# Optimization experiments

Measured on AMD Instinct MI355X. Metric: run time of the kernel, lower is better.

## Reference

```python
import jax, jax.numpy as jnp
import numpy as np

N_NODES = 4096  # nodes per graph (output1 reshaped to [-1, N_NODES])


def setup_inputs() -> dict:
    key = jax.random.key(0)
    ks = jax.random.split(key, 10)
    total_nodes = 64 * N_NODES          # 64 graphs of 4096 nodes
    n_edges = total_nodes * 8           # avg degree 8 lattice-like graph
    n_hidden = 128
    return {
        "node_features": jax.random.normal(ks[0], (total_nodes, 1), jnp.float32),
        "src": jax.random.randint(ks[1], (n_edges,), 0, total_nodes, jnp.int32),
        "dst": jax.random.randint(ks[2], (n_edges,), 0, total_nodes, jnp.int32),
        "w_self1": jax.random.normal(ks[3], (1, n_hidden), jnp.float32) * 0.5,
        "w_neigh1": jax.random.normal(ks[4], (1, n_hidden), jnp.float32) * 0.5,
        "b1": jnp.zeros((n_hidden,), jnp.float32),
        "w_self2": jax.random.normal(ks[5], (n_hidden, 1), jnp.float32) * (1.0 / np.sqrt(n_hidden)),
        "w_neigh2": jax.random.normal(ks[6], (n_hidden, 1), jnp.float32) * (1.0 / np.sqrt(n_hidden)),
        "b2": jnp.zeros((1,), jnp.float32),
        "w3": jax.random.normal(ks[7], (N_NODES, N_NODES), jnp.float32) * (1.0 / np.sqrt(N_NODES)),
        "b3": jnp.zeros((N_NODES,), jnp.float32),
    }


def _sage_mean(feat, src, dst, w_self, w_neigh, b, num_nodes):
    # gather source-node features along edges, mean-reduce at destination
    agg = jax.ops.segment_sum(feat[src], dst, num_segments=num_nodes)
    deg = jax.ops.segment_sum(jnp.ones((src.shape[0], 1), feat.dtype), dst,
                              num_segments=num_nodes)
    h_neigh = agg / jnp.maximum(deg, 1.0)
    return feat @ w_self + h_neigh @ w_neigh + b


def reference(node_features, src, dst, w_self1, w_neigh1, b1,
              w_self2, w_neigh2, b2, w3, b3):
    n = node_features.shape[0]
    h1 = jnp.tanh(_sage_mean(node_features, src, dst, w_self1, w_neigh1, b1, n))
    out1 = _sage_mean(h1, src, dst, w_self2, w_neigh2, b2, n)
    output1 = out1.reshape(-1, N_NODES)          # [batch, n_nodes]
    h2 = jnp.tanh(output1)
    output2 = h2 @ w3 + b3
    return (output1, output2)
```

## Files before the change

### kernel.cpp

```cpp
#include <hip/hip_runtime.h>


#define NTOT (64 * 4096)
#define NHID 128
#define GK   4096
#define KCH  256
#define KCHUNKS 16
#define NBINS 128
#define BSZ   2048
#define BSH   11
#define CAP   17408
#define NSL   4
#define SCB   256

typedef unsigned int u32;

__device__ __forceinline__ float fast_tanh(float x) {
    float ax = fabsf(x);
    float t  = __expf(-2.0f * ax);
    float r  = (1.0f - t) / (1.0f + t);
    return copysignf(r, x);
}


__global__ void __launch_bounds__(1024) scatter_x(const int* __restrict__ src,
                                                  const int* __restrict__ dst,
                                                  int n_edges,
                                                  int* __restrict__ edge_cnt,
                                                  u32* __restrict__ packed) {
    __shared__ int lc[NBINS];
    __shared__ int lbase[NBINS];
    int t = threadIdx.x;
    if (t < NBINS) lc[t] = 0;
    __syncthreads();
    int per = (n_edges + gridDim.x - 1) / gridDim.x;
    int e0 = blockIdx.x * per;
    int e1 = min(e0 + per, n_edges);

    int dreg[8], sreg[8];
#pragma unroll
    for (int i = 0; i < 8; ++i) {
        int e = e0 + t + i * 1024;
        bool ok = e < e1;
        int d = ok ? dst[e] : -1;
        dreg[i] = d;
        sreg[i] = ok ? src[e] : 0;
        if (ok) atomicAdd(&lc[d >> BSH], 1);
    }
    __syncthreads();
    if (t < NBINS) {
        lbase[t] = atomicAdd(&edge_cnt[t], lc[t]);
        lc[t] = 0;
    }
    __syncthreads();
#pragma unroll
    for (int i = 0; i < 8; ++i) {
        int d = dreg[i];
        if (d >= 0) {
            int b = d >> BSH;
            int pos = lbase[b] + atomicAdd(&lc[b], 1);
            if (pos < CAP)
                packed[(size_t)b * CAP + pos] =
                    ((u32)(d & (BSZ - 1)) << 18) | (u32)sreg[i];
        }
    }
}

__global__ void __launch_bounds__(1024) agg1_x(const u32* __restrict__ packed,
                                               const int* __restrict__ edge_cnt,
                                               const float* __restrict__ nf,
                                               float* __restrict__ part1) {
    __shared__ float lsum[BSZ];
    __shared__ float lcnt[BSZ];
    int t = threadIdx.x;
    int b = blockIdx.x, s = blockIdx.y;
    for (int i = t; i < BSZ; i += 1024) { lsum[i] = 0.0f; lcnt[i] = 0.0f; }
    __syncthreads();
    int en  = min(edge_cnt[b], CAP);
    int per = (en + NSL - 1) / NSL;
    int e0  = s * per;
    int e1  = min(e0 + per, en);
    const u32* pk = packed + (size_t)b * CAP;
    for (int e = e0 + t; e < e1; e += 1024) {
        u32 p = pk[e];
        int local = (int)(p >> 18);
        atomicAdd(&lsum[local], nf[p & 0x3FFFFu]);
        atomicAdd(&lcnt[local], 1.0f);
    }
    __syncthreads();
    float* dp = part1 + ((size_t)(b * NSL + s) * 2) * BSZ;
    for (int i = t; i < BSZ; i += 1024) { dp[i] = lsum[i]; dp[BSZ + i] = lcnt[i]; }
}

__global__ void node1_x(const float* __restrict__ nf, const float* __restrict__ part1,
                        const float* __restrict__ w_s1, const float* __restrict__ w_n1,
                        const float* __restrict__ bb1,
                        const float* __restrict__ w_s2, const float* __restrict__ w_n2,
                        float* __restrict__ degf, float* __restrict__ selfp,
                        float* __restrict__ sp) {
    __shared__ float lws1[NHID], lwn1[NHID], lb1[NHID], lws2[NHID], lwn2[NHID];
    int tid = threadIdx.x;
    if (tid < NHID) {
        lws1[tid] = w_s1[tid];
        lwn1[tid] = w_n1[tid];
        lb1[tid]  = bb1[tid];
        lws2[tid] = w_s2[tid];
        lwn2[tid] = w_n2[tid];
    }
    __syncthreads();
    int v = blockIdx.x * blockDim.x + tid;
    int b = v >> BSH, local = v & (BSZ - 1);
    float sum = 0.0f, cf = 0.0f;
#pragma unroll
    for (int s = 0; s < NSL; ++s) {
        const float* dp = part1 + ((size_t)(b * NSL + s) * 2) * BSZ;
        sum += dp[local];
        cf  += dp[BSZ + local];
    }
    float hn = sum / fmaxf(cf, 1.0f);
    float f = nf[v];
    float a = 0.0f, s2 = 0.0f;
#pragma unroll 8
    for (int j = 0; j < NHID; ++j) {
        float t = fast_tanh(fmaf(f, lws1[j], fmaf(hn, lwn1[j], lb1[j])));
        a  = fmaf(t, lws2[j], a);
        s2 = fmaf(t, lwn2[j], s2);
    }
    degf[v]  = cf;
    selfp[v] = a;
    sp[v]    = s2;
}

__global__ void __launch_bounds__(1024) agg2_x(const u32* __restrict__ packed,
                                               const int* __restrict__ edge_cnt,
                                               const float* __restrict__ spv,
                                               float* __restrict__ part2) {
    __shared__ float lsum[BSZ];
    int t = threadIdx.x;
    int b = blockIdx.x, s = blockIdx.y;
    for (int i = t; i < BSZ; i += 1024) lsum[i] = 0.0f;
    __syncthreads();
    int en  = min(edge_cnt[b], CAP);
    int per = (en + NSL - 1) / NSL;
    int e0  = s * per;
    int e1  = min(e0 + per, en);
    const u32* pk = packed + (size_t)b * CAP;
    for (int e = e0 + t; e < e1; e += 1024) {
        u32 p = pk[e];
        atomicAdd(&lsum[p >> 18], spv[p & 0x3FFFFu]);
    }
    __syncthreads();
    float* dp = part2 + (size_t)(b * NSL + s) * BSZ;
    for (int i = t; i < BSZ; i += 1024) dp[i] = lsum[i];
}

__global__ void node2_x(const float* __restrict__ selfp, const float* __restrict__ part2,
                        const float* __restrict__ degf, const float* __restrict__ b2p,
                        float* __restrict__ out1, float* __restrict__ h2t) {
    int v = blockIdx.x * blockDim.x + threadIdx.x;
    int b = v >> BSH, local = v & (BSZ - 1);
    float agg2 = 0.0f;
#pragma unroll
    for (int s = 0; s < NSL; ++s)
        agg2 += part2[(size_t)(b * NSL + s) * BSZ + local];
    float o = selfp[v] + agg2 / fmaxf(degf[v], 1.0f) + b2p[0];
    out1[v] = o;
    int r = v >> 12;
    int k = v & 4095;
    h2t[k * 64 + r] = fast_tanh(o);
}

__global__ void __launch_bounds__(512, 4) gemm_x(const float* __restrict__ h2t,
                                                 const float* __restrict__ w3,
                                                 float* __restrict__ Cpart) {
    int lane = threadIdx.x & 63;
    int wv   = threadIdx.x >> 6;
    int colb = blockIdx.x * 128 + lane * 2;
    int k0   = blockIdx.y * KCH;
    int row0 = __builtin_amdgcn_readfirstlane(wv * 8);

    const float* Ap = h2t + (size_t)k0 * 64 + row0;
    const float* wp = w3 + (size_t)k0 * GK + colb;

    float2 acc[8];
#pragma unroll
    for (int r = 0; r < 8; ++r) { acc[r].x = 0.0f; acc[r].y = 0.0f; }

    float2 bvA[8], bvB[8];
    float  avA[8], avB[8];

#pragma unroll
    for (int j = 0; j < 8; ++j) bvA[j] = *(const float2*)(wp + (size_t)j * GK);
#pragma unroll
    for (int r = 0; r < 8; ++r) avA[r] = Ap[r];

    for (int kk = 0; kk < KCH; kk += 16) {
#pragma unroll
        for (int j = 0; j < 8; ++j)
            bvB[j] = *(const float2*)(wp + (size_t)(kk + 8 + j) * GK);
#pragma unroll
        for (int j = 0; j < 8; ++j) {
            const float* An = Ap + (size_t)(kk + j + 1) * 64;
            float2 b = bvA[j];
            if ((j & 1) == 0) {
#pragma unroll
                for (int r = 0; r < 8; ++r) avB[r] = An[r];
#pragma unroll
                for (int r = 0; r < 8; ++r) {
                    acc[r].x = fmaf(avA[r], b.x, acc[r].x);
                    acc[r].y = fmaf(avA[r], b.y, acc[r].y);
                }
            } else {
#pragma unroll
                for (int r = 0; r < 8; ++r) avA[r] = An[r];
#pragma unroll
                for (int r = 0; r < 8; ++r) {
                    acc[r].x = fmaf(avB[r], b.x, acc[r].x);
                    acc[r].y = fmaf(avB[r], b.y, acc[r].y);
                }
            }
        }
        if (kk + 16 < KCH) {
#pragma unroll
            for (int j = 0; j < 8; ++j)
                bvA[j] = *(const float2*)(wp + (size_t)(kk + 16 + j) * GK);
        }
#pragma unroll
        for (int j = 0; j < 8; ++j) {
            int kn = kk + 8 + j + 1;
            if (kn > KCH - 1) kn = KCH - 1;
            const float* An = Ap + (size_t)kn * 64;
            float2 b = bvB[j];
            if ((j & 1) == 0) {
#pragma unroll
                for (int r = 0; r < 8; ++r) avB[r] = An[r];
#pragma unroll
                for (int r = 0; r < 8; ++r) {
                    acc[r].x = fmaf(avA[r], b.x, acc[r].x);
                    acc[r].y = fmaf(avA[r], b.y, acc[r].y);
                }
            } else {
#pragma unroll
                for (int r = 0; r < 8; ++r) avA[r] = An[r];
#pragma unroll
                for (int r = 0; r < 8; ++r) {
                    acc[r].x = fmaf(avB[r], b.x, acc[r].x);
                    acc[r].y = fmaf(avB[r], b.y, acc[r].y);
                }
            }
        }
    }

    float* Cp = Cpart + (size_t)blockIdx.y * NTOT + (size_t)row0 * GK + colb;
#pragma unroll
    for (int r = 0; r < 8; ++r) *(float2*)(Cp + (size_t)r * GK) = acc[r];
}

__global__ void reduce_x(const float4* __restrict__ Cpart, const float4* __restrict__ b3v,
                         float4* __restrict__ out2) {
    int v = blockIdx.x * blockDim.x + threadIdx.x;
    float4 s = b3v[v & 1023];
#pragma unroll
    for (int kc = 0; kc < KCHUNKS; ++kc) {
        float4 c = Cpart[(size_t)kc * (NTOT / 4) + v];
        s.x += c.x; s.y += c.y; s.z += c.z; s.w += c.w;
    }
    out2[v] = s;
}


__global__ void edge_pass1_f(const int* __restrict__ src, const int* __restrict__ dst,
                             const float* __restrict__ nf, float* __restrict__ agg,
                             float* __restrict__ deg, int n_edges) {
    int e = blockIdx.x * blockDim.x + threadIdx.x;
    if (e >= n_edges) return;
    int s = src[e], d = dst[e];
    atomicAdd(&agg[d], nf[s]);
    atomicAdd(&deg[d], 1.0f);
}

__global__ void node1_f(const float* __restrict__ nf, float* s0,
                        const float* __restrict__ deg,
                        const float* __restrict__ w_s1, const float* __restrict__ w_n1,
                        const float* __restrict__ bb1,
                        const float* __restrict__ w_s2, const float* __restrict__ w_n2,
                        float* __restrict__ sp) {
    __shared__ float lws1[NHID], lwn1[NHID], lb1[NHID], lws2[NHID], lwn2[NHID];
    int tid = threadIdx.x;
    if (tid < NHID) {
        lws1[tid] = w_s1[tid];
        lwn1[tid] = w_n1[tid];
        lb1[tid]  = bb1[tid];
        lws2[tid] = w_s2[tid];
        lwn2[tid] = w_n2[tid];
    }
    __syncthreads();
    int v = blockIdx.x * blockDim.x + tid;
    float f  = nf[v];
    float hn = s0[v] / fmaxf(deg[v], 1.0f);
    float a = 0.0f, s = 0.0f;
#pragma unroll 8
    for (int j = 0; j < NHID; ++j) {
        float t = fast_tanh(fmaf(f, lws1[j], fmaf(hn, lwn1[j], lb1[j])));
        a = fmaf(t, lws2[j], a);
        s = fmaf(t, lwn2[j], s);
    }
    s0[v] = a;
    sp[v] = s;
}

__global__ void edge_pass2_f(const int* __restrict__ src, const int* __restrict__ dst,
                             const float* __restrict__ sp, float* __restrict__ agg2,
                             int n_edges) {
    int e = blockIdx.x * blockDim.x + threadIdx.x;
    if (e >= n_edges) return;
    atomicAdd(&agg2[dst[e]], sp[src[e]]);
}

__global__ void node2_f(const float* __restrict__ s0, const float* __restrict__ agg2,
                        const float* __restrict__ deg, const float* __restrict__ b2p,
                        const float* __restrict__ b3p,
                        float* __restrict__ out1, float* __restrict__ h2t,
                        float* __restrict__ out2) {
    int v = blockIdx.x * blockDim.x + threadIdx.x;
    float o = s0[v] + agg2[v] / fmaxf(deg[v], 1.0f) + b2p[0];
    out1[v] = o;
    int r = v >> 12;
    int k = v & 4095;
    h2t[k * 64 + r] = fast_tanh(o);
    out2[v] = b3p[v & 4095];
}

__global__ void __launch_bounds__(256) gemm_f(const float* __restrict__ h2t,
                                              const float* __restrict__ w3,
                                              float* __restrict__ out2) {
    int n  = blockIdx.x * 256 + threadIdx.x;
    int k0 = blockIdx.y * KCH;
    float acc[64];
#pragma unroll
    for (int r = 0; r < 64; ++r) acc[r] = 0.0f;
    for (int k = k0; k < k0 + KCH; ++k) {
        float bv = w3[(size_t)k * GK + n];
        const float* Ak = h2t + k * 64;
#pragma unroll
        for (int r = 0; r < 64; ++r) acc[r] = fmaf(Ak[r], bv, acc[r]);
    }
#pragma unroll
    for (int r = 0; r < 64; ++r) atomicAdd(&out2[r * GK + n], acc[r]);
}


extern "C" void kernel_launch(void* const* d_in, const int* in_sizes, int n_in,
                              void* d_out, int out_size, void* d_ws, size_t ws_size,
                              hipStream_t stream) {
    const float* nf  = (const float*)d_in[0];
    const int*   src = (const int*)d_in[1];
    const int*   dst = (const int*)d_in[2];
    const float* ws1 = (const float*)d_in[3];
    const float* wn1 = (const float*)d_in[4];
    const float* b1  = (const float*)d_in[5];
    const float* ws2 = (const float*)d_in[6];
    const float* wn2 = (const float*)d_in[7];
    const float* b2  = (const float*)d_in[8];
    const float* w3  = (const float*)d_in[9];
    const float* b3  = (const float*)d_in[10];
    float* out1 = (float*)d_out;
    float* out2 = (float*)d_out + NTOT;

    int n_edges = in_sizes[1];
    int eb = (n_edges + 255) / 256;

    if (ws_size >= (size_t)20 * 1024 * 1024 && n_edges <= (1 << 21)) {
        char*  base     = (char*)d_ws;
        u32*   packed   = (u32*)base;
        float* part     = (float*)(base + 8912896);
        float* degf     = (float*)(base + 17301504);
        float* selfp    = (float*)(base + 18350080);
        float* spbuf    = (float*)(base + 19398656);
        int*   edge_cnt = (int*)(base + 20447232);
        float* h2t      = spbuf;
        float* Cpart    = (float*)base;

        (void)hipMemsetAsync(edge_cnt, 0, NBINS * sizeof(int), stream);
        scatter_x<<<SCB, 1024, 0, stream>>>(src, dst, n_edges, edge_cnt, packed);
        agg1_x<<<dim3(NBINS, NSL), 1024, 0, stream>>>(packed, edge_cnt, nf, part);
        node1_x<<<NTOT / 256, 256, 0, stream>>>(nf, part, ws1, wn1, b1, ws2, wn2,
                                                degf, selfp, spbuf);
        agg2_x<<<dim3(NBINS, NSL), 1024, 0, stream>>>(packed, edge_cnt, spbuf, part);
        node2_x<<<NTOT / 256, 256, 0, stream>>>(selfp, part, degf, b2, out1, h2t);
        gemm_x<<<dim3(GK / 128, KCHUNKS), 512, 0, stream>>>(h2t, w3, Cpart);
        reduce_x<<<NTOT / 4 / 256, 256, 0, stream>>>((const float4*)Cpart,
                                                     (const float4*)b3, (float4*)out2);
    } else {
        float* ws = (float*)d_ws;
        float* S0 = ws;
        float* S1 = ws + 1 * NTOT;
        float* S2 = ws + 2 * NTOT;
        float* S3 = ws + 3 * NTOT;

        (void)hipMemsetAsync(S0, 0, (size_t)3 * NTOT * sizeof(float), stream);
        edge_pass1_f<<<eb, 256, 0, stream>>>(src, dst, nf, S0, S1, n_edges);
        node1_f<<<NTOT / 256, 256, 0, stream>>>(nf, S0, S1, ws1, wn1, b1, ws2, wn2, S3);
        edge_pass2_f<<<eb, 256, 0, stream>>>(src, dst, S3, S2, n_edges);
        node2_f<<<NTOT / 256, 256, 0, stream>>>(S0, S2, S1, b2, b3, out1, S3, out2);
        gemm_f<<<dim3(GK / 256, KCHUNKS), 256, 0, stream>>>(S3, w3, out2);
    }
}
```

Baseline: 247.2 us.

## Stage GEMM A-tile in LDS and replace split-K reduce with atomics

The GEMM now loads its 128x64 activation slab into shared memory once per block and reads it with float4 LDS loads, instead of issuing scalar global loads per k step. The K split doubles to 32 chunks of 128, and the partial results are accumulated straight into out2 with float atomicAdd. out2 is pre-seeded with the bias in node2_x, which removes the separate reduce kernel and its partial-buffer round trip. The trade-off is heavy atomic traffic on the output, 32 adds per element, and a summation order that is no longer deterministic.

```diff
diff --git a/kernel.cpp b/kernel.cpp
--- a/kernel.cpp
+++ b/kernel.cpp
@@ -6,6 +6,8 @@
 #define GK   4096
 #define KCH  256
 #define KCHUNKS 16
+#define GKC  128
+#define GKCN 32
 #define NBINS 128
 #define BSZ   2048
 #define BSH   11
@@ -156,7 +158,9 @@
 
 __global__ void node2_x(const float* __restrict__ selfp, const float* __restrict__ part2,
                         const float* __restrict__ degf, const float* __restrict__ b2p,
-                        float* __restrict__ out1, float* __restrict__ h2t) {
+                        const float* __restrict__ b3p,
+                        float* __restrict__ out1, float* __restrict__ h2t,
+                        float* __restrict__ out2) {
     int v = blockIdx.x * blockDim.x + threadIdx.x;
     int b = v >> BSH, local = v & (BSZ - 1);
     float agg2 = 0.0f;
@@ -168,104 +172,90 @@
     int r = v >> 12;
     int k = v & 4095;
     h2t[k * 64 + r] = fast_tanh(o);
+    out2[v] = b3p[v & 4095];
 }
 
 __global__ void __launch_bounds__(512, 4) gemm_x(const float* __restrict__ h2t,
                                                  const float* __restrict__ w3,
-                                                 float* __restrict__ Cpart) {
-    int lane = threadIdx.x & 63;
-    int wv   = threadIdx.x >> 6;
+                                                 float* __restrict__ out2) {
+    __shared__ float As[GKC * 64 + 64];
+    int t    = threadIdx.x;
+    int lane = t & 63;
+    int wv   = t >> 6;
     int colb = blockIdx.x * 128 + lane * 2;
-    int k0   = blockIdx.y * KCH;
+    int k0   = blockIdx.y * GKC;
     int row0 = __builtin_amdgcn_readfirstlane(wv * 8);
 
-    const float* Ap = h2t + (size_t)k0 * 64 + row0;
-    const float* wp = w3 + (size_t)k0 * GK + colb;
+    const float4* gA = (const float4*)(h2t + (size_t)k0 * 64);
+    float4* sA = (float4*)As;
+#pragma unroll
+    for (int i = 0; i < 4; ++i) sA[t + i * 512] = gA[t + i * 512];
+
+    const float* wp  = w3 + (size_t)k0 * GK + colb;
+    const float* Asw = As + row0;
 
     float2 acc[8];
 #pragma unroll
     for (int r = 0; r < 8; ++r) { acc[r].x = 0.0f; acc[r].y = 0.0f; }
 
     float2 bvA[8], bvB[8];
-    float  avA[8], avB[8];
-
 #pragma unroll
     for (int j = 0; j < 8; ++j) bvA[j] = *(const float2*)(wp + (size_t)j * GK);
-#pragma unroll
-    for (int r = 0; r < 8; ++r) avA[r] = Ap[r];
-
-    for (int kk = 0; kk < KCH; kk += 16) {
+
+    __syncthreads();
+
+    float4 a0 = *(const float4*)(Asw);
+    float4 a1 = *(const float4*)(Asw + 4);
+
+    for (int kk = 0; kk < GKC; kk += 16) {
 #pragma unroll
         for (int j = 0; j < 8; ++j)
             bvB[j] = *(const float2*)(wp + (size_t)(kk + 8 + j) * GK);
 #pragma unroll
         for (int j = 0; j < 8; ++j) {
-            const float* An = Ap + (size_t)(kk + j + 1) * 64;
-            float2 b = bvA[j];
-            if ((j & 1) == 0) {
-#pragma unroll
-                for (int r = 0; r < 8; ++r) avB[r] = An[r];
-#pragma unroll
-                for (int r = 0; r < 8; ++r) {
-                    acc[r].x = fmaf(avA[r], b.x, acc[r].x);
-                    acc[r].y = fmaf(avA[r], b.y, acc[r].y);
-                }
-            } else {
-#pragma unroll
-                for (int r = 0; r < 8; ++r) avA[r] = An[r];
-#pragma unroll
-                for (int r = 0; r < 8; ++r) {
-                    acc[r].x = fmaf(avB[r], b.x, acc[r].x);
-                    acc[r].y = fmaf(avB[r], b.y, acc[r].y);
-                }
-            }
+            const float* An = Asw + (kk + j + 1) * 64;
+            float4 n0 = *(const float4*)(An);
+            float4 n1 = *(const float4*)(An + 4);
+            float2 b  = bvA[j];
+            acc[0].x = fmaf(a0.x, b.x, acc[0].x); acc[0].y = fmaf(a0.x, b.y, acc[0].y);
+            acc[1].x = fmaf(a0.y, b.x, acc[1].x); acc[1].y = fmaf(a0.y, b.y, acc[1].y);
+            acc[2].x = fmaf(a0.z, b.x, acc[2].x); acc[2].y = fmaf(a0.z, b.y, acc[2].y);
+            acc[3].x = fmaf(a0.w, b.x, acc[3].x); acc[3].y = fmaf(a0.w, b.y, acc[3].y);
+            acc[4].x = fmaf(a1.x, b.x, acc[4].x); acc[4].y = fmaf(a1.x, b.y, acc[4].y);
+            acc[5].x = fmaf(a1.y, b.x, acc[5].x); acc[5].y = fmaf(a1.y, b.y, acc[5].y);
+            acc[6].x = fmaf(a1.z, b.x, acc[6].x); acc[6].y = fmaf(a1.z, b.y, acc[6].y);
+            acc[7].x = fmaf(a1.w, b.x, acc[7].x); acc[7].y = fmaf(a1.w, b.y, acc[7].y);
+            a0 = n0; a1 = n1;
         }
-        if (kk + 16 < KCH) {
+        if (kk + 16 < GKC) {
 #pragma unroll
             for (int j = 0; j < 8; ++j)
                 bvA[j] = *(const float2*)(wp + (size_t)(kk + 16 + j) * GK);
         }
 #pragma unroll
         for (int j = 0; j < 8; ++j) {
-            int kn = kk + 8 + j + 1;
-            if (kn > KCH - 1) kn = KCH - 1;
-            const float* An = Ap + (size_t)kn * 64;
-            float2 b = bvB[j];
-            if ((j & 1) == 0) {
-#pragma unroll
-                for (int r = 0; r < 8; ++r) avB[r] = An[r];
-#pragma unroll
-                for (int r = 0; r < 8; ++r) {
-                    acc[r].x = fmaf(avA[r], b.x, acc[r].x);
-                    acc[r].y = fmaf(avA[r], b.y, acc[r].y);
-                }
-            } else {
-#pragma unroll
-                for (int r = 0; r < 8; ++r) avA[r] = An[r];
-#pragma unroll
-                for (int r = 0; r < 8; ++r) {
-                    acc[r].x = fmaf(avB[r], b.x, acc[r].x);
-                    acc[r].y = fmaf(avB[r], b.y, acc[r].y);
-                }
-            }
+            const float* An = Asw + (kk + 8 + j + 1) * 64;
+            float4 n0 = *(const float4*)(An);
+            float4 n1 = *(const float4*)(An + 4);
+            float2 b  = bvB[j];
+            acc[0].x = fmaf(a0.x, b.x, acc[0].x); acc[0].y = fmaf(a0.x, b.y, acc[0].y);
+            acc[1].x = fmaf(a0.y, b.x, acc[1].x); acc[1].y = fmaf(a0.y, b.y, acc[1].y);
+            acc[2].x = fmaf(a0.z, b.x, acc[2].x); acc[2].y = fmaf(a0.z, b.y, acc[2].y);
+            acc[3].x = fmaf(a0.w, b.x, acc[3].x); acc[3].y = fmaf(a0.w, b.y, acc[3].y);
+            acc[4].x = fmaf(a1.x, b.x, acc[4].x); acc[4].y = fmaf(a1.x, b.y, acc[4].y);
+            acc[5].x = fmaf(a1.y, b.x, acc[5].x); acc[5].y = fmaf(a1.y, b.y, acc[5].y);
+            acc[6].x = fmaf(a1.z, b.x, acc[6].x); acc[6].y = fmaf(a1.z, b.y, acc[6].y);
+            acc[7].x = fmaf(a1.w, b.x, acc[7].x); acc[7].y = fmaf(a1.w, b.y, acc[7].y);
+            a0 = n0; a1 = n1;
         }
     }
 
-    float* Cp = Cpart + (size_t)blockIdx.y * NTOT + (size_t)row0 * GK + colb;
-#pragma unroll
-    for (int r = 0; r < 8; ++r) *(float2*)(Cp + (size_t)r * GK) = acc[r];
-}
-
-__global__ void reduce_x(const float4* __restrict__ Cpart, const float4* __restrict__ b3v,
-                         float4* __restrict__ out2) {
-    int v = blockIdx.x * blockDim.x + threadIdx.x;
-    float4 s = b3v[v & 1023];
-#pragma unroll
-    for (int kc = 0; kc < KCHUNKS; ++kc) {
-        float4 c = Cpart[(size_t)kc * (NTOT / 4) + v];
-        s.x += c.x; s.y += c.y; s.z += c.z; s.w += c.w;
-    }
-    out2[v] = s;
+    float* Cp = out2 + (size_t)row0 * GK + colb;
+#pragma unroll
+    for (int r = 0; r < 8; ++r) {
+        atomicAdd(Cp + (size_t)r * GK,     acc[r].x);
+        atomicAdd(Cp + (size_t)r * GK + 1, acc[r].y);
+    }
 }
 
 
@@ -379,7 +369,6 @@
         float* spbuf    = (float*)(base + 19398656);
         int*   edge_cnt = (int*)(base + 20447232);
         float* h2t      = spbuf;
-        float* Cpart    = (float*)base;
 
         (void)hipMemsetAsync(edge_cnt, 0, NBINS * sizeof(int), stream);
         scatter_x<<<SCB, 1024, 0, stream>>>(src, dst, n_edges, edge_cnt, packed);
@@ -387,10 +376,9 @@
         node1_x<<<NTOT / 256, 256, 0, stream>>>(nf, part, ws1, wn1, b1, ws2, wn2,
                                                 degf, selfp, spbuf);
         agg2_x<<<dim3(NBINS, NSL), 1024, 0, stream>>>(packed, edge_cnt, spbuf, part);
-        node2_x<<<NTOT / 256, 256, 0, stream>>>(selfp, part, degf, b2, out1, h2t);
-        gemm_x<<<dim3(GK / 128, KCHUNKS), 512, 0, stream>>>(h2t, w3, Cpart);
-        reduce_x<<<NTOT / 4 / 256, 256, 0, stream>>>((const float4*)Cpart,
-                                                     (const float4*)b3, (float4*)out2);
+        node2_x<<<NTOT / 256, 256, 0, stream>>>(selfp, part, degf, b2, b3,
+                                                out1, h2t, out2);
+        gemm_x<<<dim3(GK / 128, GKCN), 512, 0, stream>>>(h2t, w3, out2);
     } else {
         float* ws = (float*)d_ws;
         float* S0 = ws;
```

New measurement: 262.4 us. +6.2%, slower.
